# Kernel optimization log

Measured on AMD Instinct MI355X. Metric: run time of the kernel, lower is better.

Reference implementation:

```python
import jax, jax.numpy as jnp
import numpy as np

M = 10          # modules per layer (args.M)
IN_DIM = 784    # 28*28
H = 20          # module width
NUM_CLASSES = 10
BATCH = 65536


def setup_inputs() -> dict:
    key = jax.random.key(0)
    ks = jax.random.split(key, 10)
    s1 = 1.0 / np.sqrt(IN_DIM)
    s2 = 1.0 / np.sqrt(H)
    return {
        "x": jax.random.normal(ks[0], (BATCH, IN_DIM), dtype=jnp.float32),
        "W1": jax.random.uniform(ks[1], (M, H, IN_DIM), jnp.float32, -s1, s1),
        "b1": jax.random.uniform(ks[2], (M, H), jnp.float32, -s1, s1),
        "W2": jax.random.uniform(ks[3], (M, H, H), jnp.float32, -s2, s2),
        "b2": jax.random.uniform(ks[4], (M, H), jnp.float32, -s2, s2),
        "W3": jax.random.uniform(ks[5], (M, H, H), jnp.float32, -s2, s2),
        "b3": jax.random.uniform(ks[6], (M, H), jnp.float32, -s2, s2),
        "Wl": jax.random.uniform(ks[7], (NUM_CLASSES, H), jnp.float32, -s2, s2),
        "bl": jax.random.uniform(ks[8], (NUM_CLASSES,), jnp.float32, -s2, s2),
        "pathway": jax.random.randint(ks[9], (3, 3), 0, M, dtype=jnp.int64),
    }


def _active(row):
    # Faithful to torch: list(set(pathway[l])) then sum_layer keeps only
    # the first element (len==1) or the sum of the first two elements.
    # CPython set of small ints iterates in sorted order.
    uniq = sorted(set(int(v) for v in np.asarray(row)))
    return np.asarray(uniq[:2], dtype=np.int64)


def _expert_layer(h, W, b, idx):
    # h: [B, F]; W[idx]: [k, H, F]; relu per module, then sum over the <=2 kept modules
    out = jax.nn.relu(jnp.einsum('bf,kof->kbo', h, W[idx]) + b[idx][:, None, :])
    return out.sum(axis=0)


def reference(x, W1, b1, W2, b2, W3, b3, Wl, bl, pathway):
    pw = np.asarray(pathway)  # pathway is static routing metadata
    i1, i2, i3 = _active(pw[0]), _active(pw[1]), _active(pw[2])
    h1 = _expert_layer(x, W1, b1, i1)    # [B, 20]
    h2 = _expert_layer(h1, W2, b2, i2)   # [B, 20]
    h3 = _expert_layer(h2, W3, b3, i3)   # [B, 20]
    return h3 @ Wl.T + bl                # [B, 10]
```

## Files before the change

### kernel.cpp

```cpp
#include <hip/hip_runtime.h>

#define BATCH   65536
#define IN_DIM  784
#define HDIM    20
#define NCLS    10
#define THREADS 256
#define SPW     16
#define SPB     64
#define NFULL   24
#define NWROWS  48

#define OFF_WHC  0
#define OFF_W2C  76800
#define OFF_W3C  79872
#define OFF_WLC  82944
#define OFF_BC   83968
#define OFF_BLC  84544

#define ABUF(b)  (smem + (size_t)(b) * 8192)
#define BBUF(b)  (smem + 32768 + (size_t)(b) * 3072)
#define WAITVM(N) asm volatile("s_waitcnt vmcnt(" #N ")" ::: "memory")

typedef __attribute__((ext_vector_type(2))) __fp16   fp16x2;
typedef __attribute__((ext_vector_type(8))) _Float16 f16x8;
typedef __attribute__((ext_vector_type(4))) float    f32x4;
typedef __attribute__((ext_vector_type(4))) unsigned u32x4;

typedef union { uint4 q; f16x8 v; } BFrag;
typedef union { fp16x2 h[4]; f16x8 v; } AFrag;
typedef union { fp16x2 h[2]; uint2 u; } Pack4;
typedef union { u32x4 u; float f[4]; } AU;
typedef union { u32x4 u; f16x8 v; } BU;

__device__ __forceinline__ void gld16(const void* g, void* l) {
    __builtin_amdgcn_global_load_lds(
        (const __attribute__((address_space(1))) unsigned int*)g,
        (__attribute__((address_space(3))) unsigned int*)l, 16, 0, 0);
}

__device__ __forceinline__ void route(const int* pw, bool is64, int row,
                                      int& e0, int& e1, float& m) {
    int v0, v1, v2;
    if (is64) {
        v0 = pw[(row * 3 + 0) * 2];
        v1 = pw[(row * 3 + 1) * 2];
        v2 = pw[(row * 3 + 2) * 2];
    } else {
        v0 = pw[row * 3 + 0];
        v1 = pw[row * 3 + 1];
        v2 = pw[row * 3 + 2];
    }
    int lo  = min(v0, min(v1, v2));
    int hi  = max(v0, max(v1, v2));
    int mid = v0 + v1 + v2 - lo - hi;
    e0 = lo;
    if (mid != lo)     { e1 = mid; m = 1.0f; }
    else if (hi != lo) { e1 = hi;  m = 1.0f; }
    else               { e1 = lo;  m = 0.0f; }
}

__global__ __launch_bounds__(256)
void cvt_w1_kernel(const float* __restrict__ W1, const int* __restrict__ pathway,
                   char* __restrict__ ws) {
    _Float16* Whc = (_Float16*)(ws + OFF_WHC);
    const int gid = blockIdx.x * 256 + threadIdx.x;
    if (gid >= NWROWS * (IN_DIM / 8)) return;
    const int u  = gid / (IN_DIM / 8);
    const int k8 = gid % (IN_DIM / 8);

    bool is64 = ((pathway[1] | pathway[3] | pathway[5] | pathway[7]) == 0);
    int e10, e11; float m1;
    route(pathway, is64, 0, e10, e11, m1);

    uint4 outw = make_uint4(0, 0, 0, 0);
    if (u < 2 * HDIM) {
        const int e = (u < HDIM) ? e10 : e11;
        const int o = (u < HDIM) ? u : u - HDIM;
        const float* src = W1 + ((size_t)e * HDIM + o) * IN_DIM + k8 * 8;
        const float4 v0 = *reinterpret_cast<const float4*>(src);
        const float4 v1 = *reinterpret_cast<const float4*>(src + 4);
        Pack4 p0, p1;
        p0.h[0] = __builtin_amdgcn_cvt_pkrtz(v0.x, v0.y);
        p0.h[1] = __builtin_amdgcn_cvt_pkrtz(v0.z, v0.w);
        p1.h[0] = __builtin_amdgcn_cvt_pkrtz(v1.x, v1.y);
        p1.h[1] = __builtin_amdgcn_cvt_pkrtz(v1.z, v1.w);
        outw = make_uint4(p0.u.x, p0.u.y, p1.u.x, p1.u.y);
    }
    *reinterpret_cast<uint4*>(Whc + (size_t)u * IN_DIM + k8 * 8) = outw;
}

__global__ __launch_bounds__(256)
void cvt_small_kernel(const float* __restrict__ W2, const float* __restrict__ W3,
                      const float* __restrict__ Wl, const float* __restrict__ b1,
                      const float* __restrict__ b2, const float* __restrict__ b3,
                      const float* __restrict__ bl, const int* __restrict__ pathway,
                      char* __restrict__ ws) {
    const int gid = blockIdx.x * 256 + threadIdx.x;
    bool is64 = ((pathway[1] | pathway[3] | pathway[5] | pathway[7]) == 0);
    int e10, e11, e20, e21, e30, e31;
    float m1, m2, m3;
    route(pathway, is64, 0, e10, e11, m1);
    route(pathway, is64, 1, e20, e21, m2);
    route(pathway, is64, 2, e30, e31, m3);

    if (gid < 1536) {
        const int u = gid >> 5, k = gid & 31;
        float v = 0.0f;
        if (u < 2 * HDIM && k < HDIM) {
            const int e = (u < HDIM) ? e20 : e21;
            const int o = (u < HDIM) ? u : u - HDIM;
            v = W2[((size_t)e * HDIM + o) * HDIM + k];
        }
        ((_Float16*)(ws + OFF_W2C))[gid] = (_Float16)v;
    } else if (gid < 3072) {
        const int i = gid - 1536;
        const int u = i >> 5, k = i & 31;
        float v = 0.0f;
        if (u < 2 * HDIM && k < HDIM) {
            const int e = (u < HDIM) ? e30 : e31;
            const int o = (u < HDIM) ? u : u - HDIM;
            v = W3[((size_t)e * HDIM + o) * HDIM + k];
        }
        ((_Float16*)(ws + OFF_W3C))[i] = (_Float16)v;
    } else if (gid < 3584) {
        const int i = gid - 3072;
        const int c = i >> 5, k = i & 31;
        float v = (c < NCLS && k < HDIM) ? Wl[c * HDIM + k] : 0.0f;
        ((_Float16*)(ws + OFF_WLC))[i] = (_Float16)v;
    } else if (gid < 3728) {
        const int i = gid - 3584;
        const int l = i / 48, hb = (i % 48) / 24, c = i % 24;
        float v = 0.0f;
        if (c < HDIM) {
            int e;
            const float* B;
            if (l == 0)      { e = hb ? e11 : e10; B = b1; }
            else if (l == 1) { e = hb ? e21 : e20; B = b2; }
            else             { e = hb ? e31 : e30; B = b3; }
            v = B[e * HDIM + c];
        }
        ((float*)(ws + OFF_BC))[i] = v;
    } else if (gid < 3744) {
        const int c = gid - 3728;
        ((float*)(ws + OFF_BLC))[c] = (c < NCLS) ? bl[c] : 0.0f;
    }
}

__device__ __forceinline__ void stageA(char* smem, int buf, int kstep,
                                       const float* __restrict__ xg,
                                       int w, int lane) {
#pragma unroll
    for (int j = 0; j < 2; ++j) {
        const int q    = w * 2 + j;
        const int row  = q * 8 + (lane >> 3);
        const int c    = (lane & 7) ^ (lane >> 3);
        const float* g = xg + (size_t)row * IN_DIM + kstep * 32 + c * 4;
        gld16(g, ABUF(buf) + q * 1024);
    }
}

__device__ __forceinline__ void stageB(char* smem, int buf, int kstep,
                                       const _Float16* __restrict__ Whc,
                                       int w, int lane) {
    if (w < 3) {
        const int row = w * 16 + (lane >> 2);
        const int c   = (lane & 3) ^ ((lane >> 3) & 3);
        const _Float16* g = Whc + (size_t)row * IN_DIM + kstep * 32 + c * 8;
        gld16(g, BBUF(buf) + w * 1024);
    }
}

__device__ __forceinline__ void computeAsm(int a0a, int a1a, int b0a, int b1a,
                                           int b2a, f32x4 acc[3]) {
    u32x4 a0, a1, b0, b1, b2;
    asm volatile("ds_read_b128 %0, %1" : "=v"(a0) : "v"(a0a));
    asm volatile("ds_read_b128 %0, %1" : "=v"(a1) : "v"(a1a));
    asm volatile("ds_read_b128 %0, %1" : "=v"(b0) : "v"(b0a));
    asm volatile("ds_read_b128 %0, %1" : "=v"(b1) : "v"(b1a));
    asm volatile("ds_read_b128 %0, %1" : "=v"(b2) : "v"(b2a));
    asm volatile("s_waitcnt lgkmcnt(0)" ::: "memory");
    __builtin_amdgcn_sched_barrier(0);
    AU ua0, ua1;
    ua0.u = a0; ua1.u = a1;
    AFrag af;
    af.h[0] = __builtin_amdgcn_cvt_pkrtz(ua0.f[0], ua0.f[1]);
    af.h[1] = __builtin_amdgcn_cvt_pkrtz(ua0.f[2], ua0.f[3]);
    af.h[2] = __builtin_amdgcn_cvt_pkrtz(ua1.f[0], ua1.f[1]);
    af.h[3] = __builtin_amdgcn_cvt_pkrtz(ua1.f[2], ua1.f[3]);
    BU ub0, ub1, ub2;
    ub0.u = b0; ub1.u = b1; ub2.u = b2;
    acc[0] = __builtin_amdgcn_mfma_f32_16x16x32_f16(af.v, ub0.v, acc[0], 0, 0, 0);
    acc[1] = __builtin_amdgcn_mfma_f32_16x16x32_f16(af.v, ub1.v, acc[1], 0, 0, 0);
    acc[2] = __builtin_amdgcn_mfma_f32_16x16x32_f16(af.v, ub2.v, acc[2], 0, 0, 0);
}

__global__ __launch_bounds__(THREADS)
void pathnet_kernel(const float* __restrict__ x, const char* __restrict__ ws,
                    const int* __restrict__ pathway, float* __restrict__ out)
{
    __shared__ __align__(16) char smem[45056];

    const int t    = threadIdx.x;
    const int lane = t & 63;
    const int w    = __builtin_amdgcn_readfirstlane(t >> 6);
    const bool wlt3 = (w < 3);

    bool is64 = ((pathway[1] | pathway[3] | pathway[5] | pathway[7]) == 0);
    int e10, e11, e20, e21, e30, e31;
    float m1, m2, m3;
    route(pathway, is64, 0, e10, e11, m1);
    route(pathway, is64, 1, e20, e21, m2);
    route(pathway, is64, 2, e30, e31, m3);

    const _Float16* Whc = (const _Float16*)(ws + OFF_WHC);
    const int sbase0 = blockIdx.x * SPB;
    const float* xg = x + (size_t)sbase0 * IN_DIM;

    const int row16 = lane & 15;
    const int kg    = lane >> 4;
    const int arow  = w * 16 + row16;
    const int aoff0 = arow * 128 + (((2 * kg + 0) ^ (arow & 7)) * 16);
    const int aoff1 = arow * 128 + (((2 * kg + 1) ^ (arow & 7)) * 16);
    int boff[3];
#pragma unroll
    for (int tt = 0; tt < 3; ++tt) {
        const int u = tt * 16 + row16;
        boff[tt] = 32768 + u * 64 + ((kg ^ ((u >> 1) & 3)) * 16);
    }

    f32x4 acc[3];
#pragma unroll
    for (int tt = 0; tt < 3; ++tt) acc[tt] = (f32x4){0.f, 0.f, 0.f, 0.f};

    stageA(smem, 0, 0, xg, w, lane);  stageB(smem, 0, 0, Whc, w, lane);
    stageA(smem, 1, 1, xg, w, lane);  stageB(smem, 1, 1, Whc, w, lane);

#pragma unroll
    for (int i = 0; i < NFULL; ++i) {
        if (i + 2 < NFULL) {
            stageA(smem, (i + 2) & 3, i + 2, xg, w, lane);
            stageB(smem, (i + 2) & 3, i + 2, Whc, w, lane);
        }
        if (i < NFULL - 2)       { if (wlt3) WAITVM(6); else WAITVM(4); }
        else if (i == NFULL - 2) { if (wlt3) WAITVM(3); else WAITVM(2); }
        else                     { WAITVM(0); }
        __builtin_amdgcn_s_barrier();
        asm volatile("" ::: "memory");
        const int bb = (i & 3);
        computeAsm(aoff0 + bb * 8192, aoff1 + bb * 8192,
                   boff[0] + bb * 3072, boff[1] + bb * 3072, boff[2] + bb * 3072,
                   acc);
    }

    {
        AFrag af;
        BFrag bf[3];
        if (kg < 2) {
            const float* ap = xg + (size_t)(w * 16 + row16) * IN_DIM + 768 + kg * 8;
            const float4 q0 = *reinterpret_cast<const float4*>(ap);
            const float4 q1 = *reinterpret_cast<const float4*>(ap + 4);
            af.h[0] = __builtin_amdgcn_cvt_pkrtz(q0.x, q0.y);
            af.h[1] = __builtin_amdgcn_cvt_pkrtz(q0.z, q0.w);
            af.h[2] = __builtin_amdgcn_cvt_pkrtz(q1.x, q1.y);
            af.h[3] = __builtin_amdgcn_cvt_pkrtz(q1.z, q1.w);
#pragma unroll
            for (int tt = 0; tt < 3; ++tt) {
                const int u = tt * 16 + row16;
                bf[tt].q = *reinterpret_cast<const uint4*>(Whc + (size_t)u * IN_DIM + 768 + kg * 8);
            }
        } else {
            const fp16x2 z = __builtin_amdgcn_cvt_pkrtz(0.f, 0.f);
            af.h[0] = af.h[1] = af.h[2] = af.h[3] = z;
#pragma unroll
            for (int tt = 0; tt < 3; ++tt) bf[tt].q = make_uint4(0, 0, 0, 0);
        }
#pragma unroll
        for (int tt = 0; tt < 3; ++tt)
            acc[tt] = __builtin_amdgcn_mfma_f32_16x16x32_f16(af.v, bf[tt].v, acc[tt], 0, 0, 0);
    }

    float* pre = reinterpret_cast<float*>(smem) + w * (16 * 44);

#pragma unroll
    for (int tt = 0; tt < 3; ++tt) {
        const int col = tt * 16 + row16;
        if (col < 2 * HDIM) {
#pragma unroll
            for (int r = 0; r < 4; ++r)
                pre[(kg * 4 + r) * 44 + col] = acc[tt][r];
        }
    }

    const _Float16* W2c = (const _Float16*)(ws + OFF_W2C);
    const _Float16* W3c = (const _Float16*)(ws + OFF_W3C);
    const _Float16* Wlc = (const _Float16*)(ws + OFF_WLC);
    const float*    bc  = (const float*)(ws + OFF_BC);
    const float*    blc = (const float*)(ws + OFF_BLC);

    BFrag w2f[3], w3f[3], wlf;
#pragma unroll
    for (int tt = 0; tt < 3; ++tt) {
        const int u = tt * 16 + row16;
        w2f[tt].q = *reinterpret_cast<const uint4*>(W2c + u * 32 + kg * 8);
        w3f[tt].q = *reinterpret_cast<const uint4*>(W3c + u * 32 + kg * 8);
    }
    wlf.q = *reinterpret_cast<const uint4*>(Wlc + row16 * 32 + kg * 8);
    const float blv = blc[row16];

    const float* prow = pre + row16 * 44;

    auto buildA = [&](const float* b0, const float* b1, float mm) -> AFrag {
        AFrag af;
        if (kg == 3) {
            const fp16x2 z = __builtin_amdgcn_cvt_pkrtz(0.f, 0.f);
            af.h[0] = af.h[1] = af.h[2] = af.h[3] = z;
            return af;
        }
        const float* p = prow + kg * 8;
        const float4 p0 = *reinterpret_cast<const float4*>(p);
        const float4 p1 = *reinterpret_cast<const float4*>(p + 4);
        const float4 q0 = *reinterpret_cast<const float4*>(p + 20);
        const float4 q1 = *reinterpret_cast<const float4*>(p + 24);
        const float4 c0 = *reinterpret_cast<const float4*>(b0 + kg * 8);
        const float4 c1 = *reinterpret_cast<const float4*>(b0 + kg * 8 + 4);
        const float4 d0 = *reinterpret_cast<const float4*>(b1 + kg * 8);
        const float4 d1 = *reinterpret_cast<const float4*>(b1 + kg * 8 + 4);
        float h[8];
        h[0] = fmaxf(p0.x + c0.x, 0.f) + mm * fmaxf(q0.x + d0.x, 0.f);
        h[1] = fmaxf(p0.y + c0.y, 0.f) + mm * fmaxf(q0.y + d0.y, 0.f);
        h[2] = fmaxf(p0.z + c0.z, 0.f) + mm * fmaxf(q0.z + d0.z, 0.f);
        h[3] = fmaxf(p0.w + c0.w, 0.f) + mm * fmaxf(q0.w + d0.w, 0.f);
        h[4] = fmaxf(p1.x + c1.x, 0.f) + mm * fmaxf(q1.x + d1.x, 0.f);
        h[5] = fmaxf(p1.y + c1.y, 0.f) + mm * fmaxf(q1.y + d1.y, 0.f);
        h[6] = fmaxf(p1.z + c1.z, 0.f) + mm * fmaxf(q1.z + d1.z, 0.f);
        h[7] = fmaxf(p1.w + c1.w, 0.f) + mm * fmaxf(q1.w + d1.w, 0.f);
        if (kg == 2) { h[4] = h[5] = h[6] = h[7] = 0.f; }
        af.h[0] = __builtin_amdgcn_cvt_pkrtz(h[0], h[1]);
        af.h[1] = __builtin_amdgcn_cvt_pkrtz(h[2], h[3]);
        af.h[2] = __builtin_amdgcn_cvt_pkrtz(h[4], h[5]);
        af.h[3] = __builtin_amdgcn_cvt_pkrtz(h[6], h[7]);
        return af;
    };

    AFrag a1 = buildA(bc + 0, bc + 24, m1);
    f32x4 acc2[3];
#pragma unroll
    for (int tt = 0; tt < 3; ++tt) {
        acc2[tt] = (f32x4){0.f, 0.f, 0.f, 0.f};
        acc2[tt] = __builtin_amdgcn_mfma_f32_16x16x32_f16(a1.v, w2f[tt].v, acc2[tt], 0, 0, 0);
    }
#pragma unroll
    for (int tt = 0; tt < 3; ++tt) {
        const int col = tt * 16 + row16;
        if (col < 2 * HDIM) {
#pragma unroll
            for (int r = 0; r < 4; ++r)
                pre[(kg * 4 + r) * 44 + col] = acc2[tt][r];
        }
    }

    AFrag a2 = buildA(bc + 48, bc + 72, m2);
    f32x4 acc3[3];
#pragma unroll
    for (int tt = 0; tt < 3; ++tt) {
        acc3[tt] = (f32x4){0.f, 0.f, 0.f, 0.f};
        acc3[tt] = __builtin_amdgcn_mfma_f32_16x16x32_f16(a2.v, w3f[tt].v, acc3[tt], 0, 0, 0);
    }
#pragma unroll
    for (int tt = 0; tt < 3; ++tt) {
        const int col = tt * 16 + row16;
        if (col < 2 * HDIM) {
#pragma unroll
            for (int r = 0; r < 4; ++r)
                pre[(kg * 4 + r) * 44 + col] = acc3[tt][r];
        }
    }

    AFrag a3 = buildA(bc + 96, bc + 120, m3);
    f32x4 accY = (f32x4){0.f, 0.f, 0.f, 0.f};
    accY = __builtin_amdgcn_mfma_f32_16x16x32_f16(a3.v, wlf.v, accY, 0, 0, 0);

    if (row16 < NCLS) {
#pragma unroll
        for (int r = 0; r < 4; ++r) {
            const int srow = sbase0 + w * SPW + kg * 4 + r;
            out[(size_t)srow * NCLS + row16] = accY[r] + blv;
        }
    }
}

extern "C" void kernel_launch(void* const* d_in, const int* in_sizes, int n_in,
                              void* d_out, int out_size, void* d_ws, size_t ws_size,
                              hipStream_t stream) {
    const float* x  = (const float*)d_in[0];
    const float* W1 = (const float*)d_in[1];
    const float* b1 = (const float*)d_in[2];
    const float* W2 = (const float*)d_in[3];
    const float* b2 = (const float*)d_in[4];
    const float* W3 = (const float*)d_in[5];
    const float* b3 = (const float*)d_in[6];
    const float* Wl = (const float*)d_in[7];
    const float* bl = (const float*)d_in[8];
    const int*   pw = (const int*)d_in[9];
    float* out = (float*)d_out;
    char* ws = (char*)d_ws;

    const int nw = NWROWS * (IN_DIM / 8);
    cvt_w1_kernel<<<(nw + 255) / 256, 256, 0, stream>>>(W1, pw, ws);
    cvt_small_kernel<<<15, 256, 0, stream>>>(W2, W3, Wl, b1, b2, b3, bl, pw, ws);

    dim3 grid(BATCH / SPB);
    pathnet_kernel<<<grid, THREADS, 0, stream>>>(x, ws, pw, out);
}
```

Baseline: 44.79 us.

## Load weight fragments directly to registers and drop per-step block barriers

The weight (B) tiles are now loaded straight from global memory into registers with global_load_dwordx4 instead of being staged through LDS. Because each wave only reads x rows it staged itself, the per-k-step s_barrier is removed. The A buffers go from four slots to three, which shrinks shared memory, and launch bounds request 4 blocks per CU to raise occupancy. Every wave now fetches the weights redundantly from cache and holds more registers, and relying on per-wave vmcnt ordering without a barrier is a correctness risk if LDS writes from global_load_lds are not visible to the same wave.

```diff
diff --git a/kernel.cpp b/kernel.cpp
--- a/kernel.cpp
+++ b/kernel.cpp
@@ -17,8 +17,7 @@
 #define OFF_BC   83968
 #define OFF_BLC  84544
 
-#define ABUF(b)  (smem + (size_t)(b) * 8192)
-#define BBUF(b)  (smem + 32768 + (size_t)(b) * 3072)
+#define PRE_OFF  24576
 #define WAITVM(N) asm volatile("s_waitcnt vmcnt(" #N ")" ::: "memory")
 
 typedef __attribute__((ext_vector_type(2))) __fp16   fp16x2;
@@ -37,6 +36,9 @@
         (const __attribute__((address_space(1))) unsigned int*)g,
         (__attribute__((address_space(3))) unsigned int*)l, 16, 0, 0);
 }
+
+#define GLOAD(dst, p) \
+    asm volatile("global_load_dwordx4 %0, %1, off" : "=&v"(dst) : "v"(p))
 
 __device__ __forceinline__ void route(const int* pw, bool is64, int row,
                                       int& e0, int& e1, float& m) {
@@ -146,64 +148,15 @@
     }
 }
 
-__device__ __forceinline__ void stageA(char* smem, int buf, int kstep,
-                                       const float* __restrict__ xg,
-                                       int w, int lane) {
-#pragma unroll
-    for (int j = 0; j < 2; ++j) {
-        const int q    = w * 2 + j;
-        const int row  = q * 8 + (lane >> 3);
-        const int c    = (lane & 7) ^ (lane >> 3);
-        const float* g = xg + (size_t)row * IN_DIM + kstep * 32 + c * 4;
-        gld16(g, ABUF(buf) + q * 1024);
-    }
-}
-
-__device__ __forceinline__ void stageB(char* smem, int buf, int kstep,
-                                       const _Float16* __restrict__ Whc,
-                                       int w, int lane) {
-    if (w < 3) {
-        const int row = w * 16 + (lane >> 2);
-        const int c   = (lane & 3) ^ ((lane >> 3) & 3);
-        const _Float16* g = Whc + (size_t)row * IN_DIM + kstep * 32 + c * 8;
-        gld16(g, BBUF(buf) + w * 1024);
-    }
-}
-
-__device__ __forceinline__ void computeAsm(int a0a, int a1a, int b0a, int b1a,
-                                           int b2a, f32x4 acc[3]) {
-    u32x4 a0, a1, b0, b1, b2;
-    asm volatile("ds_read_b128 %0, %1" : "=v"(a0) : "v"(a0a));
-    asm volatile("ds_read_b128 %0, %1" : "=v"(a1) : "v"(a1a));
-    asm volatile("ds_read_b128 %0, %1" : "=v"(b0) : "v"(b0a));
-    asm volatile("ds_read_b128 %0, %1" : "=v"(b1) : "v"(b1a));
-    asm volatile("ds_read_b128 %0, %1" : "=v"(b2) : "v"(b2a));
-    asm volatile("s_waitcnt lgkmcnt(0)" ::: "memory");
-    __builtin_amdgcn_sched_barrier(0);
-    AU ua0, ua1;
-    ua0.u = a0; ua1.u = a1;
-    AFrag af;
-    af.h[0] = __builtin_amdgcn_cvt_pkrtz(ua0.f[0], ua0.f[1]);
-    af.h[1] = __builtin_amdgcn_cvt_pkrtz(ua0.f[2], ua0.f[3]);
-    af.h[2] = __builtin_amdgcn_cvt_pkrtz(ua1.f[0], ua1.f[1]);
-    af.h[3] = __builtin_amdgcn_cvt_pkrtz(ua1.f[2], ua1.f[3]);
-    BU ub0, ub1, ub2;
-    ub0.u = b0; ub1.u = b1; ub2.u = b2;
-    acc[0] = __builtin_amdgcn_mfma_f32_16x16x32_f16(af.v, ub0.v, acc[0], 0, 0, 0);
-    acc[1] = __builtin_amdgcn_mfma_f32_16x16x32_f16(af.v, ub1.v, acc[1], 0, 0, 0);
-    acc[2] = __builtin_amdgcn_mfma_f32_16x16x32_f16(af.v, ub2.v, acc[2], 0, 0, 0);
-}
-
-__global__ __launch_bounds__(THREADS)
+__global__ __launch_bounds__(THREADS, 4)
 void pathnet_kernel(const float* __restrict__ x, const char* __restrict__ ws,
                     const int* __restrict__ pathway, float* __restrict__ out)
 {
-    __shared__ __align__(16) char smem[45056];
+    __shared__ __align__(16) char smem[PRE_OFF + 11264];
 
     const int t    = threadIdx.x;
     const int lane = t & 63;
     const int w    = __builtin_amdgcn_readfirstlane(t >> 6);
-    const bool wlt3 = (w < 3);
 
     bool is64 = ((pathway[1] | pathway[3] | pathway[5] | pathway[7]) == 0);
     int e10, e11, e20, e21, e30, e31;
@@ -216,40 +169,67 @@
     const int sbase0 = blockIdx.x * SPB;
     const float* xg = x + (size_t)sbase0 * IN_DIM;
 
+    const int srow8 = lane >> 3;
+    const int csw   = (lane & 7) ^ srow8;
+    const float* aSrc0 = xg + (size_t)((w * 2 + 0) * 8 + srow8) * IN_DIM + csw * 4;
+    const float* aSrc1 = xg + (size_t)((w * 2 + 1) * 8 + srow8) * IN_DIM + csw * 4;
+    char* aDst0 = smem + (w * 2 + 0) * 1024;
+    char* aDst1 = smem + (w * 2 + 1) * 1024;
+
     const int row16 = lane & 15;
     const int kg    = lane >> 4;
     const int arow  = w * 16 + row16;
     const int aoff0 = arow * 128 + (((2 * kg + 0) ^ (arow & 7)) * 16);
     const int aoff1 = arow * 128 + (((2 * kg + 1) ^ (arow & 7)) * 16);
-    int boff[3];
-#pragma unroll
-    for (int tt = 0; tt < 3; ++tt) {
-        const int u = tt * 16 + row16;
-        boff[tt] = 32768 + u * 64 + ((kg ^ ((u >> 1) & 3)) * 16);
-    }
+
+    const _Float16* bb0 = Whc + (size_t)(0 * 16 + row16) * IN_DIM + kg * 8;
+    const _Float16* bb1 = Whc + (size_t)(1 * 16 + row16) * IN_DIM + kg * 8;
+    const _Float16* bb2 = Whc + (size_t)(2 * 16 + row16) * IN_DIM + kg * 8;
 
     f32x4 acc[3];
 #pragma unroll
     for (int tt = 0; tt < 3; ++tt) acc[tt] = (f32x4){0.f, 0.f, 0.f, 0.f};
 
-    stageA(smem, 0, 0, xg, w, lane);  stageB(smem, 0, 0, Whc, w, lane);
-    stageA(smem, 1, 1, xg, w, lane);  stageB(smem, 1, 1, Whc, w, lane);
+    u32x4 bS[3][3];
+
+    gld16(aSrc0, aDst0);  gld16(aSrc1, aDst1);
+    GLOAD(bS[0][0], bb0); GLOAD(bS[0][1], bb1); GLOAD(bS[0][2], bb2);
+    gld16(aSrc0 + 32, aDst0 + 8192);  gld16(aSrc1 + 32, aDst1 + 8192);
+    GLOAD(bS[1][0], bb0 + 32); GLOAD(bS[1][1], bb1 + 32); GLOAD(bS[1][2], bb2 + 32);
 
 #pragma unroll
     for (int i = 0; i < NFULL; ++i) {
         if (i + 2 < NFULL) {
-            stageA(smem, (i + 2) & 3, i + 2, xg, w, lane);
-            stageB(smem, (i + 2) & 3, i + 2, Whc, w, lane);
-        }
-        if (i < NFULL - 2)       { if (wlt3) WAITVM(6); else WAITVM(4); }
-        else if (i == NFULL - 2) { if (wlt3) WAITVM(3); else WAITVM(2); }
-        else                     { WAITVM(0); }
-        __builtin_amdgcn_s_barrier();
-        asm volatile("" ::: "memory");
-        const int bb = (i & 3);
-        computeAsm(aoff0 + bb * 8192, aoff1 + bb * 8192,
-                   boff[0] + bb * 3072, boff[1] + bb * 3072, boff[2] + bb * 3072,
-                   acc);
+            const int b = (i + 2) % 3;
+            gld16(aSrc0 + (i + 2) * 32, aDst0 + b * 8192);
+            gld16(aSrc1 + (i + 2) * 32, aDst1 + b * 8192);
+            GLOAD(bS[b][0], bb0 + (i + 2) * 32);
+            GLOAD(bS[b][1], bb1 + (i + 2) * 32);
+            GLOAD(bS[b][2], bb2 + (i + 2) * 32);
+        }
+        if (i < NFULL - 2)       WAITVM(10);
+        else if (i == NFULL - 2) WAITVM(5);
+        else                     WAITVM(0);
+
+        u32x4 a0, a1;
+        const int bo = (i % 3) * 8192;
+        asm volatile("ds_read_b128 %0, %1" : "=&v"(a0) : "v"(aoff0 + bo));
+        asm volatile("ds_read_b128 %0, %1" : "=&v"(a1) : "v"(aoff1 + bo));
+        asm volatile("s_waitcnt lgkmcnt(0)" ::: "memory");
+        __builtin_amdgcn_sched_barrier(0);
+
+        AU ua0, ua1;
+        ua0.u = a0; ua1.u = a1;
+        AFrag af;
+        af.h[0] = __builtin_amdgcn_cvt_pkrtz(ua0.f[0], ua0.f[1]);
+        af.h[1] = __builtin_amdgcn_cvt_pkrtz(ua0.f[2], ua0.f[3]);
+        af.h[2] = __builtin_amdgcn_cvt_pkrtz(ua1.f[0], ua1.f[1]);
+        af.h[3] = __builtin_amdgcn_cvt_pkrtz(ua1.f[2], ua1.f[3]);
+        BU b0u, b1u, b2u;
+        b0u.u = bS[i % 3][0]; b1u.u = bS[i % 3][1]; b2u.u = bS[i % 3][2];
+        acc[0] = __builtin_amdgcn_mfma_f32_16x16x32_f16(af.v, b0u.v, acc[0], 0, 0, 0);
+        acc[1] = __builtin_amdgcn_mfma_f32_16x16x32_f16(af.v, b1u.v, acc[1], 0, 0, 0);
+        acc[2] = __builtin_amdgcn_mfma_f32_16x16x32_f16(af.v, b2u.v, acc[2], 0, 0, 0);
     }
 
     {
@@ -279,7 +259,7 @@
             acc[tt] = __builtin_amdgcn_mfma_f32_16x16x32_f16(af.v, bf[tt].v, acc[tt], 0, 0, 0);
     }
 
-    float* pre = reinterpret_cast<float*>(smem) + w * (16 * 44);
+    float* pre = reinterpret_cast<float*>(smem + PRE_OFF) + w * (16 * 44);
 
 #pragma unroll
     for (int tt = 0; tt < 3; ++tt) {
```

Measured after the change: 48.86 us. +9.1%, slower.
